# Optimization experiments

Measured on AMD Instinct MI355X. Metric: run time of the kernel, lower is better.

## Reference

```python
import jax, jax.numpy as jnp
import numpy as np

DN = ('NCHW', 'OIHW', 'NCHW')

def conv2d(x, w, pad):
    return jax.lax.conv_general_dilated(x, w, (1, 1), [(pad, pad), (pad, pad)], dimension_numbers=DN)

def conv_module(x, w, g, b):
    # Conv2d -> BN (inference-mode per-channel affine) -> ReLU
    pad = (w.shape[-1] - 1) // 2
    y = conv2d(x, w, pad)
    return jax.nn.relu(y * g[None, :, None, None] + b[None, :, None, None])

def seq_conv_module(x, w, g, b):
    # x: (T, B, C, H, W) -> apply ConvModule per frame by folding T into batch
    T, B, C, H, W = x.shape
    y = conv_module(x.reshape(T * B, C, H, W), w, g, b)
    return y.reshape(T, B, -1, H, W)

def setup_inputs() -> dict:
    key = jax.random.key(0)
    ks = jax.random.split(key, 32)
    Cin, Ck, Cv, Cout = 1024, 256, 512, 512
    T, B, H, W = 4, 1, 64, 64
    s = 0.02
    d = {}
    d['x'] = jax.random.normal(ks[0], (B, Cin, H, W), jnp.float32)
    d['seq'] = jax.random.normal(ks[1], (T, B, Cin, H, W), jnp.float32)
    def mk_cm(i, cin, cout, k):
        return (jax.random.normal(ks[i], (cout, cin, k, k), jnp.float32) * s,
                jnp.ones((cout,), jnp.float32),
                jnp.zeros((cout,), jnp.float32))
    d['wk1'], d['gk1'], d['bk1'] = mk_cm(2, Cin, Ck, 1)
    d['wk2'], d['gk2'], d['bk2'] = mk_cm(3, Ck, Ck, 3)
    d['wv1'], d['gv1'], d['bv1'] = mk_cm(4, Cin, Cv, 1)
    d['wv2'], d['gv2'], d['bv2'] = mk_cm(5, Cv, Cv, 3)
    d['wqk1'], d['gqk1'], d['bqk1'] = mk_cm(6, Cin, Ck, 1)
    d['wqk2'], d['gqk2'], d['bqk2'] = mk_cm(7, Ck, Ck, 3)
    d['wqv1'], d['gqv1'], d['bqv1'] = mk_cm(8, Cin, Cv, 1)
    d['wqv2'], d['gqv2'], d['bqv2'] = mk_cm(9, Cv, Cv, 3)
    d['wb'], d['gb'], d['bb'] = mk_cm(10, 2 * Cv, Cout, 3)
    return d

def reference(x, seq, wk1, gk1, bk1, wk2, gk2, bk2, wv1, gv1, bv1, wv2, gv2, bv2,
              wqk1, gqk1, bqk1, wqk2, gqk2, bqk2, wqv1, gqv1, bqv1, wqv2, gqv2, bqv2,
              wb, gb, bb):
    # memory key/value convs over the T reference frames
    mk = seq_conv_module(seq_conv_module(seq, wk1, gk1, bk1), wk2, gk2, bk2)  # (T,B,Ck,H,W)
    mv = seq_conv_module(seq_conv_module(seq, wv1, gv1, bv1), wv2, gv2, bv2)  # (T,B,Cv,H,W)
    # query key/value convs on current frame
    qk = conv_module(conv_module(x, wqk1, gqk1, bqk1), wqk2, gqk2, bqk2)      # (B,Ck,H,W)
    qv = conv_module(conv_module(x, wqv1, gqv1, bqv1), wqv2, gqv2, bqv2)      # (B,Cv,H,W)
    T, B, Ck, H, W = mk.shape
    Cv = mv.shape[2]
    mk = jnp.transpose(mk, (1, 2, 0, 3, 4)).reshape(B, Ck, T * H * W)         # (B,Ck,THW)
    mv = jnp.transpose(mv, (1, 2, 0, 3, 4)).reshape(B, Cv, T * H * W)         # (B,Cv,THW)
    qkf = qk.reshape(B, Ck, H * W)                                            # (B,Ck,HW)
    # attention: (B,HW,THW); matmul_norm=False so no 1/sqrt(Ck) scaling
    attn = jax.nn.softmax(jnp.einsum('bcq,bck->bqk', qkf, mk), axis=-1)
    mem = jnp.einsum('bqk,bck->bcq', attn, mv).reshape(B, Cv, H, W)
    out = conv_module(jnp.concatenate([qv, mem], axis=1), wb, gb, bb)
    return out
```

## Files before the change

### kernel.cpp

```cpp
#include <hip/hip_runtime.h>
#include <stdint.h>


typedef short bf16x8 __attribute__((ext_vector_type(8)));
typedef float f32x4  __attribute__((ext_vector_type(4)));
typedef unsigned short u16x4 __attribute__((ext_vector_type(4)));

__device__ __forceinline__ unsigned short f2bf(float f) {
  union { float f; unsigned u; } x; x.f = f;
  unsigned r = x.u + 0x7FFFu + ((x.u >> 16) & 1u);
  return (unsigned short)(r >> 16);
}

typedef const __attribute__((address_space(1))) char* as1cp;
typedef __attribute__((address_space(3))) char* as3p;

__device__ __forceinline__ void gl_lds16(const char* g, char* l) {
  __builtin_amdgcn_global_load_lds((as1cp)g, (as3p)l, 16, 0, 0);
}

enum { EP_CL_BNR = 0, EP_CF_BNR_BF16 = 1, EP_CF_BNR_F32 = 2, EP_EXPSUM = 3,
       EP_PVDIV = 4, EP_PART = 5 };

template<int EP, bool CF, bool CONV3>
__global__ __launch_bounds__(256) void gemm_k(
    const unsigned short* __restrict__ Wp,
    const unsigned short* __restrict__ Xp,
    int K, int Kc, int Xstride, int Xcoloff, int cin_log2,
    void* __restrict__ Op, int Ostride, int Ocoloff, size_t plane,
    const float* __restrict__ g1, const float* __restrict__ b1,
    const float* __restrict__ g2, const float* __restrict__ b2, int gsplit,
    float* __restrict__ rowsum, const char* __restrict__ zp)
{
  __shared__ short Wt[128 * 32];
  __shared__ short Xt[128 * 32];
  const int tid = threadIdx.x;
  const int w = tid >> 6;
  const int l = tid & 63;
  const int m0 = blockIdx.y * 128;
  const int n0 = blockIdx.x * 128;
  const int wrow0 = CF ? n0 : m0;
  const int xrow0 = CF ? m0 : n0;

  const int ch0 = w, ch1 = w + 4;
  const int sr0 = ch0 * 16 + (l >> 2);
  const int sr1 = ch1 * 16 + (l >> 2);
  const int kbp = (l & 3) << 4;
  const int kbl0 = kbp ^ ((sr0 & 3) << 4);
  const int kbl1 = kbp ^ ((sr1 & 3) << 4);

  const size_t wrb = (size_t)K * 2;
  const size_t xrb = (size_t)Xstride * 2;

  const short* At = CF ? Xt : Wt;
  const short* Bt = CF ? Wt : Xt;
  const int wm = (w >> 1) * 64;
  const int wn = (w & 1) * 64;

  const int k_begin = blockIdx.z * Kc;
  const int k_end = (k_begin + Kc < K) ? (k_begin + Kc) : K;

  f32x4 acc[4][4] = {};

  for (int k0 = k_begin; k0 < k_end; k0 += 32) {
    int ci0 = k0, kh = 1, kw = 1, dpos = 0;
    if (CONV3) {
      int e = k0 >> cin_log2;
      ci0 = k0 & ((1 << cin_log2) - 1);
      kh = e / 3; kw = e - kh * 3;
      dpos = (kh - 1) * 64 + (kw - 1);
    }
    __syncthreads();
    gl_lds16((const char*)Wp + (size_t)(wrow0 + sr0) * wrb + (size_t)k0 * 2 + kbl0,
             (char*)Wt + ch0 * 1024);
    gl_lds16((const char*)Wp + (size_t)(wrow0 + sr1) * wrb + (size_t)k0 * 2 + kbl1,
             (char*)Wt + ch1 * 1024);
    const char* xs0;
    const char* xs1;
    if (CONV3) {
      int p = xrow0 + sr0;
      int hw = p & 4095;
      int h2 = (hw >> 6) + kh - 1, w2 = (hw & 63) + kw - 1;
      xs0 = ((unsigned)h2 < 64u && (unsigned)w2 < 64u)
          ? (const char*)Xp + (size_t)(p + dpos) * xrb + (size_t)(Xcoloff + ci0) * 2 + kbl0
          : zp + kbl0;
      p = xrow0 + sr1;
      hw = p & 4095;
      h2 = (hw >> 6) + kh - 1; w2 = (hw & 63) + kw - 1;
      xs1 = ((unsigned)h2 < 64u && (unsigned)w2 < 64u)
          ? (const char*)Xp + (size_t)(p + dpos) * xrb + (size_t)(Xcoloff + ci0) * 2 + kbl1
          : zp + kbl1;
    } else {
      xs0 = (const char*)Xp + (size_t)(xrow0 + sr0) * xrb + (size_t)(Xcoloff + k0) * 2 + kbl0;
      xs1 = (const char*)Xp + (size_t)(xrow0 + sr1) * xrb + (size_t)(Xcoloff + k0) * 2 + kbl1;
    }
    gl_lds16(xs0, (char*)Xt + ch0 * 1024);
    gl_lds16(xs1, (char*)Xt + ch1 * 1024);
    __syncthreads();

    bf16x8 af[4], bfv[4];
#pragma unroll
    for (int i = 0; i < 4; i++) {
      int row = wm + i * 16 + (l & 15);
      int kb = ((l >> 4) << 4) ^ ((row & 3) << 4);
      af[i] = *(const bf16x8*)(At + row * 32 + (kb >> 1));
    }
#pragma unroll
    for (int j = 0; j < 4; j++) {
      int row = wn + j * 16 + (l & 15);
      int kb = ((l >> 4) << 4) ^ ((row & 3) << 4);
      bfv[j] = *(const bf16x8*)(Bt + row * 32 + (kb >> 1));
    }
#pragma unroll
    for (int i = 0; i < 4; i++)
#pragma unroll
      for (int j = 0; j < 4; j++)
        acc[i][j] = __builtin_amdgcn_mfma_f32_16x16x32_bf16(af[i], bfv[j], acc[i][j], 0, 0, 0);
  }

  const int col = l & 15;
  const int rb = (l >> 4) << 2;

  if constexpr (EP == EP_PART) {
    float* P = (float*)Op + (size_t)blockIdx.z * plane;
#pragma unroll
    for (int j = 0; j < 4; j++) {
      int gn = n0 + wn + j * 16 + col;
#pragma unroll
      for (int i = 0; i < 4; i++) {
        int gm = m0 + wm + i * 16 + rb;
        *(f32x4*)(P + (size_t)gn * Ostride + gm) = acc[i][j];
      }
    }
  }
  if constexpr (EP == EP_CL_BNR) {
#pragma unroll
    for (int i = 0; i < 4; i++) {
      int gm = m0 + wm + i * 16 + rb;
      const float* gp; const float* bp;
      if (gm < gsplit) { gp = g1 + gm; bp = b1 + gm; }
      else             { gp = g2 + (gm - gsplit); bp = b2 + (gm - gsplit); }
      float G[4], B[4];
#pragma unroll
      for (int r = 0; r < 4; r++) { G[r] = gp[r]; B[r] = bp[r]; }
#pragma unroll
      for (int j = 0; j < 4; j++) {
        int gn = n0 + wn + j * 16 + col;
        f32x4 v = acc[i][j];
        u16x4 o;
#pragma unroll
        for (int r = 0; r < 4; r++) o[r] = f2bf(fmaxf(v[r] * G[r] + B[r], 0.f));
        *(u16x4*)((unsigned short*)Op + (size_t)gn * Ostride + Ocoloff + gm) = o;
      }
    }
  }
  if constexpr (EP == EP_CF_BNR_BF16 || EP == EP_CF_BNR_F32) {
#pragma unroll
    for (int j = 0; j < 4; j++) {
      int gn = n0 + wn + j * 16 + col;
      float G = (gn < gsplit) ? g1[gn] : g2[gn - gsplit];
      float Bv = (gn < gsplit) ? b1[gn] : b2[gn - gsplit];
#pragma unroll
      for (int i = 0; i < 4; i++) {
        int gm = m0 + wm + i * 16 + rb;
        f32x4 v = acc[i][j];
        if constexpr (EP == EP_CF_BNR_F32) {
          f32x4 o;
#pragma unroll
          for (int r = 0; r < 4; r++) o[r] = fmaxf(v[r] * G + Bv, 0.f);
          *(f32x4*)((float*)Op + (size_t)gn * Ostride + Ocoloff + gm) = o;
        } else {
          u16x4 o;
#pragma unroll
          for (int r = 0; r < 4; r++) o[r] = f2bf(fmaxf(v[r] * G + Bv, 0.f));
          *(u16x4*)((unsigned short*)Op + (size_t)gn * Ostride + Ocoloff + gm) = o;
        }
      }
    }
  }
  if constexpr (EP == EP_EXPSUM) {
#pragma unroll
    for (int j = 0; j < 4; j++) {
      int gn = n0 + wn + j * 16 + col;
      float s = 0.f;
#pragma unroll
      for (int i = 0; i < 4; i++) {
        int gm = m0 + wm + i * 16 + rb;
        f32x4 v = acc[i][j];
        u16x4 o;
#pragma unroll
        for (int r = 0; r < 4; r++) { float e = __expf(v[r]); s += e; o[r] = f2bf(e); }
        *(u16x4*)((unsigned short*)Op + (size_t)gn * Ostride + gm) = o;
      }
      s += __shfl_xor(s, 16);
      s += __shfl_xor(s, 32);
      if (l < 16) atomicAdd(rowsum + gn, s);
    }
  }
  if constexpr (EP == EP_PVDIV) {
#pragma unroll
    for (int j = 0; j < 4; j++) {
      int gn = n0 + wn + j * 16 + col;
      float inv = 1.0f / rowsum[gn];
#pragma unroll
      for (int i = 0; i < 4; i++) {
        int gm = m0 + wm + i * 16 + rb;
        f32x4 v = acc[i][j];
        u16x4 o;
#pragma unroll
        for (int r = 0; r < 4; r++) o[r] = f2bf(v[r] * inv);
        *(u16x4*)((unsigned short*)Op + (size_t)gn * Ostride + Ocoloff + gm) = o;
      }
    }
  }
}

enum { RED_BNR_BF16 = 0, RED_PVDIV = 1, RED_BNR_F32 = 2 };

template<int MODE>
__global__ __launch_bounds__(256) void reduce_k(
    const float* __restrict__ P, int Z, size_t plane, int Cdim,
    void* __restrict__ out, int Ostride, int Ocoloff,
    const float* __restrict__ g1, const float* __restrict__ b1,
    const float* __restrict__ g2, const float* __restrict__ b2, int gsplit,
    const float* __restrict__ rowsum, int total4)
{
  int t = blockIdx.x * 256 + threadIdx.x;
  if (t >= total4) return;
  size_t base = (size_t)t * 4;
  int n = (int)(base / (size_t)Cdim);
  int c = (int)(base % (size_t)Cdim);
  f32x4 s = *(const f32x4*)(P + base);
  for (int z = 1; z < Z; z++) {
    f32x4 v = *(const f32x4*)(P + (size_t)z * plane + base);
    s += v;
  }
  if constexpr (MODE == RED_BNR_BF16) {
    u16x4 o;
#pragma unroll
    for (int r = 0; r < 4; r++) {
      int ch = c + r;
      float G = (ch < gsplit) ? g1[ch] : g2[ch - gsplit];
      float B = (ch < gsplit) ? b1[ch] : b2[ch - gsplit];
      o[r] = f2bf(fmaxf(s[r] * G + B, 0.f));
    }
    *(u16x4*)((unsigned short*)out + (size_t)n * Ostride + Ocoloff + c) = o;
  }
  if constexpr (MODE == RED_PVDIV) {
    float inv = 1.0f / rowsum[n];
    u16x4 o;
#pragma unroll
    for (int r = 0; r < 4; r++) o[r] = f2bf(s[r] * inv);
    *(u16x4*)((unsigned short*)out + (size_t)n * Ostride + Ocoloff + c) = o;
  }
  if constexpr (MODE == RED_BNR_F32) {
    float G = g1[n], B = b1[n];
    f32x4 o;
#pragma unroll
    for (int r = 0; r < 4; r++) o[r] = fmaxf(s[r] * G + B, 0.f);
    *(f32x4*)((float*)out + (size_t)n * Ostride + c) = o;
  }
}

__global__ __launch_bounds__(256) void nchw_to_cl(const float* __restrict__ src,
                                                  unsigned short* __restrict__ dst,
                                                  int C, int P) {
  __shared__ float t[32][33];
  int f = blockIdx.z;
  src += (size_t)f * C * P;
  dst += (size_t)f * C * P;
  int p0 = blockIdx.x * 32, c0 = blockIdx.y * 32;
  int a = threadIdx.x & 31, b = threadIdx.x >> 5;
#pragma unroll
  for (int k = 0; k < 4; k++)
    t[b + 8 * k][a] = src[(size_t)(c0 + b + 8 * k) * P + p0 + a];
  __syncthreads();
#pragma unroll
  for (int k = 0; k < 4; k++)
    dst[(size_t)(p0 + b + 8 * k) * C + c0 + a] = f2bf(t[a][b + 8 * k]);
}

__global__ __launch_bounds__(256) void cvt_bf16(const float* __restrict__ s,
                                                unsigned short* __restrict__ d, int n) {
  int i = blockIdx.x * 256 + threadIdx.x;
  if (i < n) d[i] = f2bf(s[i]);
}

__global__ __launch_bounds__(256) void repack3(const float* __restrict__ s,
                                               unsigned short* __restrict__ d,
                                               int ci_log2, int n) {
  int i = blockIdx.x * 256 + threadIdx.x;
  if (i >= n) return;
  int Ci = 1 << ci_log2;
  int ci = i & (Ci - 1);
  int t = i >> ci_log2;
  int e = t % 9;
  int co = t / 9;
  d[i] = f2bf(s[((size_t)co * Ci + ci) * 9 + e]);
}

__global__ __launch_bounds__(256) void fillf(float* p, float v, int n) {
  int i = blockIdx.x * 256 + threadIdx.x;
  if (i < n) p[i] = v;
}

extern "C" void kernel_launch(void* const* d_in, const int* in_sizes, int n_in,
                              void* d_out, int out_size, void* d_ws, size_t ws_size,
                              hipStream_t stream) {
  (void)in_sizes; (void)n_in;
  const float* x    = (const float*)d_in[0];
  const float* seq  = (const float*)d_in[1];
  const float* wk1  = (const float*)d_in[2];
  const float* gk1  = (const float*)d_in[3];
  const float* bk1  = (const float*)d_in[4];
  const float* wk2  = (const float*)d_in[5];
  const float* gk2  = (const float*)d_in[6];
  const float* bk2  = (const float*)d_in[7];
  const float* wv1  = (const float*)d_in[8];
  const float* gv1  = (const float*)d_in[9];
  const float* bv1  = (const float*)d_in[10];
  const float* wv2  = (const float*)d_in[11];
  const float* gv2  = (const float*)d_in[12];
  const float* bv2  = (const float*)d_in[13];
  const float* wqk1 = (const float*)d_in[14];
  const float* gqk1 = (const float*)d_in[15];
  const float* bqk1 = (const float*)d_in[16];
  const float* wqk2 = (const float*)d_in[17];
  const float* gqk2 = (const float*)d_in[18];
  const float* bqk2 = (const float*)d_in[19];
  const float* wqv1 = (const float*)d_in[20];
  const float* gqv1 = (const float*)d_in[21];
  const float* bqv1 = (const float*)d_in[22];
  const float* wqv2 = (const float*)d_in[23];
  const float* gqv2 = (const float*)d_in[24];
  const float* bqv2 = (const float*)d_in[25];
  const float* wb   = (const float*)d_in[26];
  const float* gb   = (const float*)d_in[27];
  const float* bb   = (const float*)d_in[28];

  char* ws = (char*)d_ws;
  size_t off = 0;
  auto alloc = [&](size_t bytes) { size_t o = off; off += (bytes + 255) & ~(size_t)255; return o; };
  size_t o_zp    = alloc(4096);
  size_t o_rs    = alloc(4096 * 4);
  size_t o_wKV1  = alloc((size_t)768 * 1024 * 2);
  size_t o_wQKV1 = alloc((size_t)768 * 1024 * 2);
  size_t o_wK2   = alloc((size_t)256 * 2304 * 2);
  size_t o_wQK2  = alloc((size_t)256 * 2304 * 2);
  size_t o_wV2   = alloc((size_t)512 * 4608 * 2);
  size_t o_wQV2  = alloc((size_t)512 * 4608 * 2);
  size_t o_wB    = alloc((size_t)512 * 9216 * 2);
  size_t o_mk    = alloc((size_t)16384 * 256 * 2);
  size_t o_mv    = alloc((size_t)512 * 16384 * 2);
  size_t o_qk    = alloc((size_t)4096 * 256 * 2);
  size_t o_qvm   = alloc((size_t)4096 * 1024 * 2);
  size_t o_part  = alloc((size_t)8 * 4096 * 512 * 4);
  size_t o_vol   = off;
  size_t o_xT    = o_vol;
  size_t o_seqT  = o_xT + (size_t)4096 * 1024 * 2;
  size_t o_kv1   = o_seqT + (size_t)4 * 4096 * 1024 * 2;
  size_t o_qkv1  = o_kv1 + (size_t)16384 * 768 * 2;
  size_t end1    = o_qkv1 + (size_t)4096 * 768 * 2;
  size_t o_expS  = o_vol;
  size_t end2    = o_expS + (size_t)4096 * 16384 * 2;
  size_t need    = end1 > end2 ? end1 : end2;

  bool SPLIT = ws_size >= need;
  if (!SPLIT) {
    size_t save = o_part;
    o_vol  = save;
    o_xT   = o_vol;
    o_seqT = o_xT + (size_t)4096 * 1024 * 2;
    o_kv1  = o_seqT + (size_t)4 * 4096 * 1024 * 2;
    o_qkv1 = o_kv1 + (size_t)16384 * 768 * 2;
    end1   = o_qkv1 + (size_t)4096 * 768 * 2;
    o_expS = o_vol;
    end2   = o_expS + (size_t)4096 * 16384 * 2;
    need   = end1 > end2 ? end1 : end2;
    if (ws_size < need) {
      fillf<<<(out_size + 255) / 256, 256, 0, stream>>>((float*)d_out, 12345.0f, out_size);
      return;
    }
  }

  const char* zp = ws + o_zp;
  float* rs = (float*)(ws + o_rs);
  unsigned short* wKV1p  = (unsigned short*)(ws + o_wKV1);
  unsigned short* wQKV1p = (unsigned short*)(ws + o_wQKV1);
  unsigned short* wK2p   = (unsigned short*)(ws + o_wK2);
  unsigned short* wQK2p  = (unsigned short*)(ws + o_wQK2);
  unsigned short* wV2p   = (unsigned short*)(ws + o_wV2);
  unsigned short* wQV2p  = (unsigned short*)(ws + o_wQV2);
  unsigned short* wBp    = (unsigned short*)(ws + o_wB);
  unsigned short* mkp    = (unsigned short*)(ws + o_mk);
  unsigned short* mvp    = (unsigned short*)(ws + o_mv);
  unsigned short* qkp    = (unsigned short*)(ws + o_qk);
  unsigned short* qvmp   = (unsigned short*)(ws + o_qvm);
  float* partp           = (float*)(ws + o_part);
  unsigned short* xTp    = (unsigned short*)(ws + o_xT);
  unsigned short* seqTp  = (unsigned short*)(ws + o_seqT);
  unsigned short* kv1p   = (unsigned short*)(ws + o_kv1);
  unsigned short* qkv1p  = (unsigned short*)(ws + o_qkv1);
  unsigned short* expSp  = (unsigned short*)(ws + o_expS);

  hipMemsetAsync(ws + o_zp, 0, 4096, stream);
  hipMemsetAsync(ws + o_rs, 0, 4096 * 4, stream);

  cvt_bf16<<<(256 * 1024 + 255) / 256, 256, 0, stream>>>(wk1, wKV1p, 256 * 1024);
  cvt_bf16<<<(512 * 1024 + 255) / 256, 256, 0, stream>>>(wv1, wKV1p + 256 * 1024, 512 * 1024);
  cvt_bf16<<<(256 * 1024 + 255) / 256, 256, 0, stream>>>(wqk1, wQKV1p, 256 * 1024);
  cvt_bf16<<<(512 * 1024 + 255) / 256, 256, 0, stream>>>(wqv1, wQKV1p + 256 * 1024, 512 * 1024);
  repack3<<<(256 * 2304 + 255) / 256, 256, 0, stream>>>(wk2, wK2p, 8, 256 * 2304);
  repack3<<<(256 * 2304 + 255) / 256, 256, 0, stream>>>(wqk2, wQK2p, 8, 256 * 2304);
  repack3<<<(512 * 4608 + 255) / 256, 256, 0, stream>>>(wv2, wV2p, 9, 512 * 4608);
  repack3<<<(512 * 4608 + 255) / 256, 256, 0, stream>>>(wqv2, wQV2p, 9, 512 * 4608);
  repack3<<<(512 * 9216 + 255) / 256, 256, 0, stream>>>(wb, wBp, 10, 512 * 9216);

  nchw_to_cl<<<dim3(128, 32, 1), 256, 0, stream>>>(x, xTp, 1024, 4096);
  nchw_to_cl<<<dim3(128, 32, 4), 256, 0, stream>>>(seq, seqTp, 1024, 4096);

  gemm_k<EP_CL_BNR, false, false><<<dim3(128, 6), 256, 0, stream>>>(
      wKV1p, seqTp, 1024, 1024, 1024, 0, 0, kv1p, 768, 0, 0,
      gk1, bk1, gv1, bv1, 256, rs, zp);
  if (SPLIT) {
    size_t plane = (size_t)4096 * 768;
    gemm_k<EP_PART, false, false><<<dim3(32, 6, 2), 256, 0, stream>>>(
        wQKV1p, xTp, 1024, 512, 1024, 0, 0, partp, 768, 0, plane,
        nullptr, nullptr, nullptr, nullptr, 0, rs, zp);
    int t4 = (int)(plane / 4);
    reduce_k<RED_BNR_BF16><<<(t4 + 255) / 256, 256, 0, stream>>>(
        partp, 2, plane, 768, qkv1p, 768, 0, gqk1, bqk1, gqv1, bqv1, 256, rs, t4);
  } else {
    gemm_k<EP_CL_BNR, false, false><<<dim3(32, 6), 256, 0, stream>>>(
        wQKV1p, xTp, 1024, 1024, 1024, 0, 0, qkv1p, 768, 0, 0,
        gqk1, bqk1, gqv1, bqv1, 256, rs, zp);
  }

  gemm_k<EP_CL_BNR, false, true><<<dim3(128, 2), 256, 0, stream>>>(
      wK2p, kv1p, 2304, 2304, 768, 0, 8, mkp, 256, 0, 0,
      gk2, bk2, gk2, bk2, 256, rs, zp);
  if (SPLIT) {
    size_t plane = (size_t)4096 * 256;
    gemm_k<EP_PART, false, true><<<dim3(32, 2, 4), 256, 0, stream>>>(
        wQK2p, qkv1p, 2304, 576, 768, 0, 8, partp, 256, 0, plane,
        nullptr, nullptr, nullptr, nullptr, 0, rs, zp);
    int t4 = (int)(plane / 4);
    reduce_k<RED_BNR_BF16><<<(t4 + 255) / 256, 256, 0, stream>>>(
        partp, 4, plane, 256, qkp, 256, 0, gqk2, bqk2, gqk2, bqk2, 256, rs, t4);
  } else {
    gemm_k<EP_CL_BNR, false, true><<<dim3(32, 2), 256, 0, stream>>>(
        wQK2p, qkv1p, 2304, 2304, 768, 0, 8, qkp, 256, 0, 0,
        gqk2, bqk2, gqk2, bqk2, 256, rs, zp);
  }
  if (SPLIT) {
    size_t plane = (size_t)4096 * 512;
    gemm_k<EP_PART, false, true><<<dim3(32, 4, 4), 256, 0, stream>>>(
        wQV2p, qkv1p, 4608, 1152, 768, 256, 9, partp, 512, 0, plane,
        nullptr, nullptr, nullptr, nullptr, 0, rs, zp);
    int t4 = (int)(plane / 4);
    reduce_k<RED_BNR_BF16><<<(t4 + 255) / 256, 256, 0, stream>>>(
        partp, 4, plane, 512, qvmp, 1024, 0, gqv2, bqv2, gqv2, bqv2, 512, rs, t4);
  } else {
    gemm_k<EP_CL_BNR, false, true><<<dim3(32, 4), 256, 0, stream>>>(
        wQV2p, qkv1p, 4608, 4608, 768, 256, 9, qvmp, 1024, 0, 0,
        gqv2, bqv2, gqv2, bqv2, 512, rs, zp);
  }
  gemm_k<EP_CF_BNR_BF16, true, true><<<dim3(4, 128), 256, 0, stream>>>(
      wV2p, kv1p, 4608, 4608, 768, 256, 9, mvp, 16384, 0, 0,
      gv2, bv2, gv2, bv2, 512, rs, zp);

  gemm_k<EP_EXPSUM, false, false><<<dim3(32, 128), 256, 0, stream>>>(
      mkp, qkp, 256, 256, 256, 0, 0, expSp, 16384, 0, 0,
      nullptr, nullptr, nullptr, nullptr, 1 << 30, rs, zp);
  if (SPLIT) {
    size_t plane = (size_t)4096 * 512;
    gemm_k<EP_PART, false, false><<<dim3(32, 4, 8), 256, 0, stream>>>(
        mvp, expSp, 16384, 2048, 16384, 0, 0, partp, 512, 0, plane,
        nullptr, nullptr, nullptr, nullptr, 0, rs, zp);
    int t4 = (int)(plane / 4);
    reduce_k<RED_PVDIV><<<(t4 + 255) / 256, 256, 0, stream>>>(
        partp, 8, plane, 512, qvmp, 1024, 512, nullptr, nullptr, nullptr, nullptr, 0, rs, t4);
  } else {
    gemm_k<EP_PVDIV, false, false><<<dim3(32, 4), 256, 0, stream>>>(
        mvp, expSp, 16384, 16384, 16384, 0, 0, qvmp, 1024, 512, 0,
        nullptr, nullptr, nullptr, nullptr, 1 << 30, rs, zp);
  }

  if (SPLIT) {
    size_t plane = (size_t)512 * 4096;
    gemm_k<EP_PART, true, true><<<dim3(4, 32, 4), 256, 0, stream>>>(
        wBp, qvmp, 9216, 2304, 1024, 0, 10, partp, 4096, 0, plane,
        nullptr, nullptr, nullptr, nullptr, 0, rs, zp);
    int t4 = (int)(plane / 4);
    reduce_k<RED_BNR_F32><<<(t4 + 255) / 256, 256, 0, stream>>>(
        partp, 4, plane, 4096, (float*)d_out, 4096, 0, gb, bb, gb, bb, 512, rs, t4);
  } else {
    gemm_k<EP_CF_BNR_F32, true, true><<<dim3(4, 32), 256, 0, stream>>>(
        wBp, qvmp, 9216, 9216, 1024, 0, 10, (float*)d_out, 4096, 0, 0,
        gb, bb, gb, bb, 512, rs, zp);
  }
}
```

Measured before the change: 673.4 us.

## Double-buffer LDS tiles to overlap global loads with MFMA compute

The GEMM main loop now uses two LDS buffers for the weight and activation tiles. It issues the async global-to-LDS loads for the next K-step before computing on the current one, and uses an explicit vmcnt wait with barriers in place of the two __syncthreads per step. This is meant to hide global memory latency behind the MFMA work. In exchange it doubles shared memory per block, which may lower occupancy, and it depends on the exact vmcnt count of outstanding loads being correct.

```diff
diff --git a/kernel.cpp b/kernel.cpp
--- a/kernel.cpp
+++ b/kernel.cpp
@@ -32,8 +32,8 @@
     const float* __restrict__ g2, const float* __restrict__ b2, int gsplit,
     float* __restrict__ rowsum, const char* __restrict__ zp)
 {
-  __shared__ short Wt[128 * 32];
-  __shared__ short Xt[128 * 32];
+  __shared__ short Wt[2][128 * 32];
+  __shared__ short Xt[2][128 * 32];
   const int tid = threadIdx.x;
   const int w = tid >> 6;
   const int l = tid & 63;
@@ -52,17 +52,13 @@
   const size_t wrb = (size_t)K * 2;
   const size_t xrb = (size_t)Xstride * 2;
 
-  const short* At = CF ? Xt : Wt;
-  const short* Bt = CF ? Wt : Xt;
   const int wm = (w >> 1) * 64;
   const int wn = (w & 1) * 64;
 
   const int k_begin = blockIdx.z * Kc;
   const int k_end = (k_begin + Kc < K) ? (k_begin + Kc) : K;
 
-  f32x4 acc[4][4] = {};
-
-  for (int k0 = k_begin; k0 < k_end; k0 += 32) {
+  auto stage = [&](int b, int k0) {
     int ci0 = k0, kh = 1, kw = 1, dpos = 0;
     if (CONV3) {
       int e = k0 >> cin_log2;
@@ -70,11 +66,12 @@
       kh = e / 3; kw = e - kh * 3;
       dpos = (kh - 1) * 64 + (kw - 1);
     }
-    __syncthreads();
+    char* Wl = (char*)&Wt[b][0];
+    char* Xl = (char*)&Xt[b][0];
     gl_lds16((const char*)Wp + (size_t)(wrow0 + sr0) * wrb + (size_t)k0 * 2 + kbl0,
-             (char*)Wt + ch0 * 1024);
+             Wl + ch0 * 1024);
     gl_lds16((const char*)Wp + (size_t)(wrow0 + sr1) * wrb + (size_t)k0 * 2 + kbl1,
-             (char*)Wt + ch1 * 1024);
+             Wl + ch1 * 1024);
     const char* xs0;
     const char* xs1;
     if (CONV3) {
@@ -94,9 +91,27 @@
       xs0 = (const char*)Xp + (size_t)(xrow0 + sr0) * xrb + (size_t)(Xcoloff + k0) * 2 + kbl0;
       xs1 = (const char*)Xp + (size_t)(xrow0 + sr1) * xrb + (size_t)(Xcoloff + k0) * 2 + kbl1;
     }
-    gl_lds16(xs0, (char*)Xt + ch0 * 1024);
-    gl_lds16(xs1, (char*)Xt + ch1 * 1024);
-    __syncthreads();
+    gl_lds16(xs0, Xl + ch0 * 1024);
+    gl_lds16(xs1, Xl + ch1 * 1024);
+  };
+
+  f32x4 acc[4][4] = {};
+
+  int cur = 0;
+  stage(0, k_begin);
+  for (int k0 = k_begin; k0 < k_end; k0 += 32) {
+    if (k0 + 32 < k_end) {
+      stage(cur ^ 1, k0 + 32);
+      asm volatile("s_waitcnt vmcnt(4)" ::: "memory");
+    } else {
+      asm volatile("s_waitcnt vmcnt(0)" ::: "memory");
+    }
+    __builtin_amdgcn_s_barrier();
+
+    const short* Wb = &Wt[cur][0];
+    const short* Xb = &Xt[cur][0];
+    const short* At = CF ? Xb : Wb;
+    const short* Bt = CF ? Wb : Xb;
 
     bf16x8 af[4], bfv[4];
 #pragma unroll
@@ -116,6 +131,9 @@
 #pragma unroll
       for (int j = 0; j < 4; j++)
         acc[i][j] = __builtin_amdgcn_mfma_f32_16x16x32_bf16(af[i], bfv[j], acc[i][j], 0, 0, 0);
+
+    __builtin_amdgcn_s_barrier();
+    cur ^= 1;
   }
 
   const int col = l & 15;
```

After: 646.3 us. 1.04x faster.
